# Performance work log

Measured on AMD Instinct MI355X. Metric: run time of the kernel, lower is better.

Reference implementation:

```python
import jax, jax.numpy as jnp
import numpy as np

B, T, C = 8, 512, 2048          # batch streams, qlen, hidden_size
H, Z = 32, 64                   # num_heads, head_size; A = H*Z = attention_hidden_size
A = H * Z
TMX, TDX = 32, 64               # TIME_MIX_EXTRA_DIM, TIME_DECAY_EXTRA_DIM
EPS = 1e-5 * 8.0**2             # ln_x eps = 1e-5 * head_size_divisor**2


def setup_inputs() -> dict:
    key = jax.random.key(0)
    ks = jax.random.split(key, 24)
    def rn(i, shape, scale=1.0):
        return jax.random.normal(ks[i], shape, jnp.float32) * scale
    inv_c = 1.0 / np.sqrt(C)
    return {
        "hidden_states": rn(0, (B * T, C)),
        "positions": jnp.zeros((B * T,), jnp.int32),
        "input_kv_state": jnp.zeros((B, H, Z, Z), jnp.float32),
        "input_shift_state": rn(1, (B, C)),
        "time_maa_x": rn(2, (1, 1, C), 0.1),
        "time_maa_w": rn(3, (1, 1, C), 0.1),
        "time_maa_k": rn(4, (1, 1, C), 0.1),
        "time_maa_v": rn(5, (1, 1, C), 0.1),
        "time_maa_r": rn(6, (1, 1, C), 0.1),
        "time_maa_g": rn(7, (1, 1, C), 0.1),
        "time_maa_w1": rn(8, (C, TMX * 5), inv_c),
        "time_maa_w2": rn(9, (5, TMX, C), 1.0 / np.sqrt(TMX)),
        "time_decay": rn(10, (1, 1, A), 0.5),
        "time_decay_w1": rn(11, (C, TDX), inv_c),
        "time_decay_w2": rn(12, (TDX, A), 0.01),
        "time_faaaa": rn(13, (H, Z), 0.1),
        "W_r": rn(14, (C, A), inv_c),
        "W_k": rn(15, (C, A), inv_c),
        "W_v": rn(16, (C, A), inv_c),
        "W_g": rn(17, (C, A), inv_c),
        "W_o": rn(18, (A, C), inv_c),
        "ln_w": 1.0 + rn(19, (C,), 0.1),
        "ln_b": rn(20, (C,), 0.1),
    }


def _rwkv6_forward(hidden_states, positions, input_kv_state, input_shift_state,
                   time_maa_x, time_maa_w, time_maa_k, time_maa_v, time_maa_r,
                   time_maa_g, time_maa_w1, time_maa_w2, time_decay,
                   time_decay_w1, time_decay_w2, time_faaaa,
                   W_r, W_k, W_v, W_g, W_o, ln_w, ln_b):
    x = hidden_states.reshape(B, T, C)
    pos0_is_zero = positions.reshape(B, T)[:, 0] == 0
    reset = jnp.where(pos0_is_zero, -100.0, 0.0)  # [B]
    # kill shift state for fresh sequences (matches * exp(-100))
    shift = input_shift_state * jnp.exp(reset)[:, None]  # [B, C]

    # token-shift mixing (shift state broadcast over T, as in source)
    xx = shift[:, None, :] - x  # [B, T, C]
    xxx = x + xx * time_maa_x
    mix = jnp.tanh(xxx @ time_maa_w1).reshape(B, T, 5, TMX)
    mix = jnp.einsum('btfe,fec->fbtc', mix, time_maa_w2)  # [5, B, T, C]
    mw, mk, mv, mr, mg = mix

    td_in = x + xx * (time_maa_w + mw)
    kx = x + xx * (time_maa_k + mk)
    vx = x + xx * (time_maa_v + mv)
    rx = x + xx * (time_maa_r + mr)
    gx = x + xx * (time_maa_g + mg)

    r = rx @ W_r
    k = kx @ W_k
    v = vx @ W_v
    g = jax.nn.silu(gx @ W_g)  # [B, T, A]

    w = time_decay + jnp.tanh(td_in @ time_decay_w1) @ time_decay_w2
    w = -jnp.exp(w.astype(jnp.float32))  # log-decay, [B, T, A]

    # split heads -> [T, B, H, Z] for scan
    def to_tbhz(a):
        return a.reshape(B, T, H, Z).transpose(1, 0, 2, 3)
    r_s, k_s, v_s, w_s = to_tbhz(r), to_tbhz(k), to_tbhz(v), to_tbhz(w)
    # zero out carried state at t=0 for fresh sequences
    w_s = w_s.at[0].add(reset[:, None, None])

    u = time_faaaa  # [H, Z]

    def step(S, rkvw):
        # S: [B, H, K, V] (key-dim x value-dim state)
        r_t, k_t, v_t, w_t = rkvw  # each [B, H, Z]
        kv = k_t[..., :, None] * v_t[..., None, :]  # [B, H, K, V]
        o = jnp.einsum('bhk,bhkv->bhv', r_t, S + u[None, :, :, None] * kv)
        S = jnp.exp(w_t)[..., None] * S + kv
        return S, o

    S_out, o = jax.lax.scan(step, input_kv_state, (r_s, k_s, v_s, w_s))
    xo = o.transpose(1, 0, 2, 3).reshape(B * T, C)  # [B*T, C]

    # GroupNorm over heads (num_groups = H)
    xg = xo.reshape(B * T, H, Z)
    mu = xg.mean(-1, keepdims=True)
    var = xg.var(-1, keepdims=True)
    xn = ((xg - mu) * jax.lax.rsqrt(var + EPS)).reshape(B * T, C) * ln_w + ln_b

    out = (xn.reshape(B, T, C) * g) @ W_o  # [B, T, C]
    return out.reshape(B * T, C)


def reference(hidden_states, positions, input_kv_state, input_shift_state,
              time_maa_x, time_maa_w, time_maa_k, time_maa_v, time_maa_r,
              time_maa_g, time_maa_w1, time_maa_w2, time_decay,
              time_decay_w1, time_decay_w2, time_faaaa,
              W_r, W_k, W_v, W_g, W_o, ln_w, ln_b):
    return _rwkv6_forward(hidden_states, positions, input_kv_state,
                          input_shift_state, time_maa_x, time_maa_w,
                          time_maa_k, time_maa_v, time_maa_r, time_maa_g,
                          time_maa_w1, time_maa_w2, time_decay, time_decay_w1,
                          time_decay_w2, time_faaaa, W_r, W_k, W_v, W_g, W_o,
                          ln_w, ln_b)
```

## Files before the change

### kernel.cpp

```cpp
#include <hip/hip_runtime.h>
#include <cmath>

#define NB 8
#define NT 512
#define NC 2048
#define NH 32
#define NZ 64
static constexpr float GN_EPS = 1e-5f * 64.0f;

typedef _Float16 f16;
typedef __attribute__((ext_vector_type(8))) _Float16 f16x8;
typedef __attribute__((ext_vector_type(4))) _Float16 f16x4;
typedef __attribute__((ext_vector_type(4))) float f4;

static __device__ __forceinline__ void gload16(const void* gp, void* lp) {
  __builtin_amdgcn_global_load_lds(
      (const __attribute__((address_space(1))) void*)gp,
      (__attribute__((address_space(3))) void*)lp, 16, 0, 0);
}

__global__ void k_transpose_cast(const float* __restrict__ in, f16* __restrict__ out,
                                 int R, int Cc) {
  __shared__ float tile[32][33];
  int c0 = blockIdx.x * 32, r0 = blockIdx.y * 32;
  int tx = threadIdx.x, ty = threadIdx.y;
#pragma unroll
  for (int i = 0; i < 4; ++i)
    tile[ty + i * 8][tx] = in[(size_t)(r0 + ty + i * 8) * Cc + c0 + tx];
  __syncthreads();
#pragma unroll
  for (int i = 0; i < 4; ++i)
    out[(size_t)(c0 + ty + i * 8) * R + r0 + tx] = (f16)tile[tx][ty + i * 8];
}

__global__ void k_transpose_split(const float* __restrict__ in, f16* __restrict__ ohi,
                                  f16* __restrict__ olo, int R, int Cc) {
  __shared__ float tile[32][33];
  int c0 = blockIdx.x * 32, r0 = blockIdx.y * 32;
  int tx = threadIdx.x, ty = threadIdx.y;
#pragma unroll
  for (int i = 0; i < 4; ++i)
    tile[ty + i * 8][tx] = in[(size_t)(r0 + ty + i * 8) * Cc + c0 + tx];
  __syncthreads();
#pragma unroll
  for (int i = 0; i < 4; ++i) {
    float v = tile[tx][ty + i * 8];
    f16 h = (f16)v;
    size_t o = (size_t)(c0 + ty + i * 8) * R + r0 + tx;
    ohi[o] = h;
    olo[o] = (f16)(v - (float)h);
  }
}

__global__ void k_xxx(const float* __restrict__ hs, const float* __restrict__ shift_st,
                      const int* __restrict__ positions, const float* __restrict__ maa_x,
                      float* __restrict__ xxx) {
  int i = blockIdx.x * blockDim.x + threadIdx.x;
  int idx = i * 4;
  int c = idx & (NC - 1);
  int t = idx >> 11;
  int b = t >> 9;
  float er = (positions[b * NT] == 0) ? expf(-100.0f) : 1.0f;
  const float4 x = *(const float4*)(hs + idx);
  const float4 sh = *(const float4*)(shift_st + b * NC + c);
  const float4 mx = *(const float4*)(maa_x + c);
  float4 o;
  o.x = x.x + (sh.x * er - x.x) * mx.x;
  o.y = x.y + (sh.y * er - x.y) * mx.y;
  o.z = x.z + (sh.z * er - x.z) * mx.z;
  o.w = x.w + (sh.w * er - x.w) * mx.w;
  *(float4*)(xxx + idx) = o;
}

static __device__ __forceinline__ void split4(const float4 v, int base, f16x8& hi, f16x8& lo) {
  float x[4] = {v.x, v.y, v.z, v.w};
#pragma unroll
  for (int j = 0; j < 4; ++j) {
    f16 h = (f16)x[j];
    hi[base + j] = h;
    lo[base + j] = (f16)(x[j] - (float)h);
  }
}

__global__ __launch_bounds__(64) void k_mix1_split(const float* __restrict__ A,
                                                   const f16* __restrict__ Bhi,
                                                   const f16* __restrict__ Blo,
                                                   float* __restrict__ out) {
  int m0 = blockIdx.x * 16, n0 = blockIdx.y * 16;
  int lane = threadIdx.x, lr = lane & 15, kq = lane >> 4;
  f4 acc = {0.f, 0.f, 0.f, 0.f};
  const float* ap = A + (size_t)(m0 + lr) * 2048 + kq * 8;
  const f16* bh0 = Bhi + (size_t)(n0 + lr) * 2048 + kq * 8;
  const f16* bl0 = Blo + (size_t)(n0 + lr) * 2048 + kq * 8;
  for (int k0 = 0; k0 < 2048; k0 += 32) {
    f16x8 ah, al;
    split4(*(const float4*)(ap + k0), 0, ah, al);
    split4(*(const float4*)(ap + k0 + 4), 4, ah, al);
    f16x8 bh = *(const f16x8*)(bh0 + k0);
    f16x8 bl = *(const f16x8*)(bl0 + k0);
    acc = __builtin_amdgcn_mfma_f32_16x16x32_f16(ah, bh, acc, 0, 0, 0);
    acc = __builtin_amdgcn_mfma_f32_16x16x32_f16(ah, bl, acc, 0, 0, 0);
    acc = __builtin_amdgcn_mfma_f32_16x16x32_f16(al, bh, acc, 0, 0, 0);
  }
#pragma unroll
  for (int r = 0; r < 4; ++r)
    out[(size_t)(m0 + kq * 4 + r) * 160 + n0 + lr] = tanhf(acc[r]);
}

__global__ __launch_bounds__(64) void k_tmp5_split(const float* __restrict__ mixb,
    const f16* __restrict__ Bhi, const f16* __restrict__ Blo,
    const float* __restrict__ hs, const float* __restrict__ shift_st,
    const int* __restrict__ positions,
    const float* __restrict__ maa_w, const float* __restrict__ maa_k,
    const float* __restrict__ maa_v, const float* __restrict__ maa_r,
    const float* __restrict__ maa_g,
    float* __restrict__ tdin, f16* __restrict__ kx, f16* __restrict__ vx,
    f16* __restrict__ rx, f16* __restrict__ gx) {
  int m0 = blockIdx.x * 16, n0 = blockIdx.y * 16;
  int lane = threadIdx.x, lr = lane & 15, kq = lane >> 4;
  f4 acc[5];
#pragma unroll
  for (int f = 0; f < 5; ++f) acc[f] = (f4){0.f, 0.f, 0.f, 0.f};
  const float* ap = mixb + (size_t)(m0 + lr) * 160 + kq * 8;
#pragma unroll
  for (int f = 0; f < 5; ++f) {
    f16x8 ah, al;
    split4(*(const float4*)(ap + f * 32), 0, ah, al);
    split4(*(const float4*)(ap + f * 32 + 4), 4, ah, al);
    size_t bi = ((size_t)f * 2048 + n0 + lr) * 32 + kq * 8;
    f16x8 bh = *(const f16x8*)(Bhi + bi);
    f16x8 bl = *(const f16x8*)(Blo + bi);
    acc[f] = __builtin_amdgcn_mfma_f32_16x16x32_f16(ah, bh, acc[f], 0, 0, 0);
    acc[f] = __builtin_amdgcn_mfma_f32_16x16x32_f16(ah, bl, acc[f], 0, 0, 0);
    acc[f] = __builtin_amdgcn_mfma_f32_16x16x32_f16(al, bh, acc[f], 0, 0, 0);
  }
  int c = n0 + lr;
  float mw = maa_w[c], mk = maa_k[c], mv = maa_v[c], mr = maa_r[c], mg = maa_g[c];
#pragma unroll
  for (int r = 0; r < 4; ++r) {
    int t = m0 + kq * 4 + r;
    int b = t >> 9;
    float er = (positions[b * NT] == 0) ? expf(-100.0f) : 1.0f;
    float x = hs[(size_t)t * NC + c];
    float xxv = shift_st[b * NC + c] * er - x;
    size_t oi = (size_t)t * NC + c;
    tdin[oi] = x + xxv * (mw + acc[0][r]);
    kx[oi] = (f16)(x + xxv * (mk + acc[1][r]));
    vx[oi] = (f16)(x + xxv * (mv + acc[2][r]));
    rx[oi] = (f16)(x + xxv * (mr + acc[3][r]));
    gx[oi] = (f16)(x + xxv * (mg + acc[4][r]));
  }
}

__global__ __launch_bounds__(64) void k_wd1_split(const float* __restrict__ A,
                                                  const f16* __restrict__ Bhi,
                                                  const f16* __restrict__ Blo,
                                                  float* __restrict__ out) {
  int m0 = blockIdx.x * 16, n0 = blockIdx.y * 16;
  int lane = threadIdx.x, lr = lane & 15, kq = lane >> 4;
  f4 acc = {0.f, 0.f, 0.f, 0.f};
  const float* ap = A + (size_t)(m0 + lr) * 2048 + kq * 8;
  const f16* bh0 = Bhi + (size_t)(n0 + lr) * 2048 + kq * 8;
  const f16* bl0 = Blo + (size_t)(n0 + lr) * 2048 + kq * 8;
  for (int k0 = 0; k0 < 2048; k0 += 32) {
    f16x8 ah, al;
    split4(*(const float4*)(ap + k0), 0, ah, al);
    split4(*(const float4*)(ap + k0 + 4), 4, ah, al);
    f16x8 bh = *(const f16x8*)(bh0 + k0);
    f16x8 bl = *(const f16x8*)(bl0 + k0);
    acc = __builtin_amdgcn_mfma_f32_16x16x32_f16(ah, bh, acc, 0, 0, 0);
    acc = __builtin_amdgcn_mfma_f32_16x16x32_f16(ah, bl, acc, 0, 0, 0);
    acc = __builtin_amdgcn_mfma_f32_16x16x32_f16(al, bh, acc, 0, 0, 0);
  }
#pragma unroll
  for (int r = 0; r < 4; ++r)
    out[(size_t)(m0 + kq * 4 + r) * 64 + n0 + lr] = tanhf(acc[r]);
}

__global__ __launch_bounds__(64) void k_wdecay_split(const float* __restrict__ A,
                                                     const f16* __restrict__ Bhi,
                                                     const f16* __restrict__ Blo,
                                                     const float* __restrict__ time_decay,
                                                     float* __restrict__ wout) {
  int m0 = blockIdx.x * 16, n0 = blockIdx.y * 16;
  int lane = threadIdx.x, lr = lane & 15, kq = lane >> 4;
  f4 acc = {0.f, 0.f, 0.f, 0.f};
#pragma unroll
  for (int kk = 0; kk < 2; ++kk) {
    f16x8 ah, al;
    const float* ap = A + (size_t)(m0 + lr) * 64 + kk * 32 + kq * 8;
    split4(*(const float4*)ap, 0, ah, al);
    split4(*(const float4*)(ap + 4), 4, ah, al);
    size_t bi = (size_t)(n0 + lr) * 64 + kk * 32 + kq * 8;
    f16x8 bh = *(const f16x8*)(Bhi + bi);
    f16x8 bl = *(const f16x8*)(Blo + bi);
    acc = __builtin_amdgcn_mfma_f32_16x16x32_f16(ah, bh, acc, 0, 0, 0);
    acc = __builtin_amdgcn_mfma_f32_16x16x32_f16(ah, bl, acc, 0, 0, 0);
    acc = __builtin_amdgcn_mfma_f32_16x16x32_f16(al, bh, acc, 0, 0, 0);
  }
  int c = n0 + lr;
  float td = time_decay[c];
#pragma unroll
  for (int r = 0; r < 4; ++r) {
    int t = m0 + kq * 4 + r;
    wout[(size_t)t * NC + c] = -expf(td + acc[r]);
  }
}

#define GBM 128
#define GBN 128
#define GBK 64

template <int EPI>
__global__ __launch_bounds__(256) void k_gemm_big(const f16* __restrict__ A,
                                                  const f16* __restrict__ Bt,
                                                  float* __restrict__ Cf,
                                                  f16* __restrict__ Cb, int K) {
  __shared__ __align__(16) f16 As[2][GBM][GBK];
  __shared__ __align__(16) f16 Bs[2][GBN][GBK];
  int nwg = gridDim.x * gridDim.y;
  int wg = blockIdx.y * gridDim.x + blockIdx.x;
  int swz = (wg & 7) * (nwg >> 3) + (wg >> 3);
  int n0 = (swz % gridDim.x) * GBN;
  int m0 = (swz / gridDim.x) * GBM;
  int tid = threadIdx.x;
  int wid = tid >> 6, lane = tid & 63;
  int wr = wid >> 1, wc = wid & 1;
  int lr = lane & 15, kq = lane >> 4;
  int sw = lr & 7;
  int gunit = (lane & 7) ^ (lane >> 3);
  const f16* aL = A + (size_t)(m0 + wid * 32 + (lane >> 3)) * K + gunit * 8;
  const f16* bL = Bt + (size_t)(n0 + wid * 32 + (lane >> 3)) * K + gunit * 8;
  f4 acc[4][4];
#pragma unroll
  for (int m = 0; m < 4; ++m)
#pragma unroll
    for (int n = 0; n < 4; ++n) acc[m][n] = (f4){0.f, 0.f, 0.f, 0.f};

#pragma unroll
  for (int i = 0; i < 4; ++i) {
    gload16(aL + (size_t)i * 8 * K, &As[0][wid * 32 + i * 8][0]);
    gload16(bL + (size_t)i * 8 * K, &Bs[0][wid * 32 + i * 8][0]);
  }
  __syncthreads();
  int niter = K / GBK;
  int cur = 0;
  for (int it = 0; it < niter; ++it) {
    if (it + 1 < niter) {
      int k0 = (it + 1) * GBK;
#pragma unroll
      for (int i = 0; i < 4; ++i) {
        gload16(aL + k0 + (size_t)i * 8 * K, &As[cur ^ 1][wid * 32 + i * 8][0]);
        gload16(bL + k0 + (size_t)i * 8 * K, &Bs[cur ^ 1][wid * 32 + i * 8][0]);
      }
    }
#pragma unroll
    for (int kk = 0; kk < 2; ++kk) {
      f16x8 af[4], bfv[4];
      int un = ((kk * 4 + kq) ^ sw) * 8;
#pragma unroll
      for (int m = 0; m < 4; ++m)
        af[m] = *(const f16x8*)&As[cur][wr * 64 + m * 16 + lr][un];
#pragma unroll
      for (int n = 0; n < 4; ++n)
        bfv[n] = *(const f16x8*)&Bs[cur][wc * 64 + n * 16 + lr][un];
#pragma unroll
      for (int m = 0; m < 4; ++m)
#pragma unroll
        for (int n = 0; n < 4; ++n)
          acc[m][n] = __builtin_amdgcn_mfma_f32_16x16x32_f16(af[m], bfv[n], acc[m][n], 0, 0, 0);
    }
    __syncthreads();
    cur ^= 1;
  }
#pragma unroll
  for (int m = 0; m < 4; ++m) {
    int row0 = m0 + wr * 64 + m * 16 + kq * 4;
#pragma unroll
    for (int n = 0; n < 4; ++n) {
      int col = n0 + wc * 64 + n * 16 + lr;
#pragma unroll
      for (int r = 0; r < 4; ++r) {
        float v = acc[m][n][r];
        size_t oi = (size_t)(row0 + r) * NC + col;
        if (EPI == 0) {
          Cf[oi] = v;
        } else {
          float s = v / (1.0f + expf(-v));
          Cb[oi] = (f16)s;
        }
      }
    }
  }
}

__global__ __launch_bounds__(64) void k_scanB(
    const float* rb, const float* __restrict__ kb,
    const float* __restrict__ vb, const float* __restrict__ wb,
    const float* __restrict__ kvstate, const int* __restrict__ positions,
    const float* __restrict__ faaaa, f16* __restrict__ o,
    float* rtil, float* __restrict__ Ebuf, float* __restrict__ Dbuf) {
  int blk = blockIdx.x;
  int bh = blk >> 3, c = blk & 7;
  int b = bh >> 5, h = bh & 31;
  int zz = threadIdx.x;
  __shared__ __align__(16) float shR[64];
  __shared__ __align__(16) float shE[64];
  __shared__ __align__(16) float shK[64];
  float S[64];
  if (c == 0) {
    const float* S0 = kvstate + (size_t)bh * 4096;
#pragma unroll
    for (int j = 0; j < 64; ++j) S[j] = S0[j * 64 + zz];
  } else {
#pragma unroll
    for (int j = 0; j < 64; ++j) S[j] = 0.f;
  }
  float u = faaaa[h * 64 + zz];
  float reset = (positions[b * NT] == 0) ? -100.0f : 0.0f;
  const size_t base = ((size_t)(b * NT) + c * 64) * NC + h * 64 + zz;
  float vr = rb[base], vk = kb[base], vw = wb[base], vv = vb[base];
  float Pw = 1.0f;
  for (int t = 0; t < 64; ++t) {
    float nr = 0.f, nk = 0.f, nw = 0.f, nv = 0.f;
    if (t + 1 < 64) {
      size_t idx = base + (size_t)(t + 1) * NC;
      nr = rb[idx]; nk = kb[idx]; nw = wb[idx]; nv = vb[idx];
    }
    float ww = vw;
    if (c == 0 && t == 0) ww += reset;
    float ew = expf(ww);
    shR[zz] = vr; shE[zz] = ew; shK[zz] = vk;
    float q = vr * u * vk;
    q += __shfl_xor(q, 1);  q += __shfl_xor(q, 2);  q += __shfl_xor(q, 4);
    q += __shfl_xor(q, 8);  q += __shfl_xor(q, 16); q += __shfl_xor(q, 32);
    __syncthreads();
    if (c > 0) rtil[base + (size_t)t * NC] = vr * Pw;
    Pw *= ew;
    float oacc = vv * q;
#pragma unroll
    for (int k0 = 0; k0 < 64; k0 += 4) {
      f4 r4 = *(const f4*)&shR[k0];
      f4 e4 = *(const f4*)&shE[k0];
      f4 k4 = *(const f4*)&shK[k0];
#pragma unroll
      for (int j = 0; j < 4; ++j) {
        oacc = fmaf(r4[j], S[k0 + j], oacc);
        S[k0 + j] = fmaf(e4[j], S[k0 + j], k4[j] * vv);
      }
    }
    o[base + (size_t)t * NC] = (f16)oacc;
    __syncthreads();
    vr = nr; vk = nk; vw = nw; vv = nv;
  }
  if (c < 7) {
    float* E = Ebuf + ((size_t)bh * 7 + c) * 4096;
#pragma unroll
    for (int j = 0; j < 64; ++j) E[j * 64 + zz] = S[j];
  }
  Dbuf[((size_t)bh * 8 + c) * 64 + zz] = Pw;
}

__global__ __launch_bounds__(256) void k_comb(float* __restrict__ Ebuf,
                                              const float* __restrict__ Dbuf) {
  int bh = blockIdx.x, tid = threadIdx.x;
  int k = tid >> 2, v0 = (tid & 3) * 16;
  float* base = Ebuf + (size_t)bh * 7 * 4096;
  float S[16];
#pragma unroll
  for (int j = 0; j < 16; ++j) S[j] = base[k * 64 + v0 + j];
  for (int c = 2; c <= 7; ++c) {
    float d = Dbuf[((size_t)bh * 8 + (c - 1)) * 64 + k];
    float* slot = base + (size_t)(c - 1) * 4096;
#pragma unroll
    for (int j = 0; j < 16; ++j) {
      S[j] = fmaf(d, S[j], slot[k * 64 + v0 + j]);
      slot[k * 64 + v0 + j] = S[j];
    }
  }
}

__global__ __launch_bounds__(256) void k_fix(const float* __restrict__ rtil,
                                             const float* __restrict__ Ebuf,
                                             f16* __restrict__ o) {
  int blk = blockIdx.x;
  int bh = blk / 7, cm = blk - bh * 7;
  int c = cm + 1;
  int b = bh >> 5, h = bh & 31;
  __shared__ float Rs[64][65];
  __shared__ float Ss[64][65];
  int tid = threadIdx.x;
  const float* rsrc = rtil + ((size_t)(b * NT) + c * 64) * NC + h * NZ;
  const float* ssrc = Ebuf + ((size_t)bh * 7 + cm) * 4096;
#pragma unroll
  for (int q = 0; q < 4; ++q) {
    int li = tid * 4 + q;
    int rr = li >> 4, cc = (li & 15) * 4;
    float4 x = *(const float4*)(rsrc + (size_t)rr * NC + cc);
    Rs[rr][cc] = x.x; Rs[rr][cc + 1] = x.y; Rs[rr][cc + 2] = x.z; Rs[rr][cc + 3] = x.w;
    float4 y = *(const float4*)(ssrc + rr * 64 + cc);
    Ss[rr][cc] = y.x; Ss[rr][cc + 1] = y.y; Ss[rr][cc + 2] = y.z; Ss[rr][cc + 3] = y.w;
  }
  __syncthreads();
  int t = tid >> 2, v0 = (tid & 3) * 16;
  float acc[16];
#pragma unroll
  for (int j = 0; j < 16; ++j) acc[j] = 0.f;
  for (int k = 0; k < 64; ++k) {
    float rv = Rs[t][k];
#pragma unroll
    for (int j = 0; j < 16; ++j) acc[j] = fmaf(rv, Ss[k][v0 + j], acc[j]);
  }
  f16* op = o + ((size_t)(b * NT) + c * 64 + t) * NC + h * NZ + v0;
  f16x8 o0 = *(f16x8*)op, o1 = *(f16x8*)(op + 8);
#pragma unroll
  for (int j = 0; j < 8; ++j) {
    o0[j] = (f16)((float)o0[j] + acc[j]);
    o1[j] = (f16)((float)o1[j] + acc[j + 8]);
  }
  *(f16x8*)op = o0;
  *(f16x8*)(op + 8) = o1;
}

__global__ __launch_bounds__(256) void k_gnorm(const f16* __restrict__ xo, const f16* __restrict__ g,
    const float* __restrict__ ln_w, const float* __restrict__ ln_b, f16* __restrict__ y) {
  int t = blockIdx.x;
  int tid = threadIdx.x;
  int c = tid * 8;
  f16x8 xv8 = *(const f16x8*)(xo + (size_t)t * NC + c);
  float xv[8];
#pragma unroll
  for (int j = 0; j < 8; ++j) xv[j] = (float)xv8[j];
  float s = 0.f, ss = 0.f;
#pragma unroll
  for (int j = 0; j < 8; ++j) { s += xv[j]; ss += xv[j] * xv[j]; }
  s += __shfl_xor(s, 1); ss += __shfl_xor(ss, 1);
  s += __shfl_xor(s, 2); ss += __shfl_xor(ss, 2);
  s += __shfl_xor(s, 4); ss += __shfl_xor(ss, 4);
  float mu = s * (1.0f / 64.0f);
  float var = ss * (1.0f / 64.0f) - mu * mu;
  float rstd = rsqrtf(var + GN_EPS);
  f16x8 gv = *(const f16x8*)(g + (size_t)t * NC + c);
  f16x8 ov;
#pragma unroll
  for (int j = 0; j < 8; ++j) {
    float xn = (xv[j] - mu) * rstd * ln_w[c + j] + ln_b[c + j];
    ov[j] = (f16)(xn * (float)gv[j]);
  }
  *(f16x8*)(y + (size_t)t * NC + c) = ov;
}

extern "C" void kernel_launch(void* const* d_in, const int* in_sizes, int n_in,
                              void* d_out, int out_size, void* d_ws, size_t ws_size,
                              hipStream_t stream) {
  const float* hs = (const float*)d_in[0];
  const int* positions = (const int*)d_in[1];
  const float* kvstate = (const float*)d_in[2];
  const float* shift_st = (const float*)d_in[3];
  const float* maa_x = (const float*)d_in[4];
  const float* maa_w = (const float*)d_in[5];
  const float* maa_k = (const float*)d_in[6];
  const float* maa_v = (const float*)d_in[7];
  const float* maa_r = (const float*)d_in[8];
  const float* maa_g = (const float*)d_in[9];
  const float* maa_w1 = (const float*)d_in[10];
  const float* maa_w2 = (const float*)d_in[11];
  const float* time_decay = (const float*)d_in[12];
  const float* decay_w1 = (const float*)d_in[13];
  const float* decay_w2 = (const float*)d_in[14];
  const float* faaaa = (const float*)d_in[15];
  const float* W_r = (const float*)d_in[16];
  const float* W_k = (const float*)d_in[17];
  const float* W_v = (const float*)d_in[18];
  const float* W_g = (const float*)d_in[19];
  const float* W_o = (const float*)d_in[20];
  const float* ln_w = (const float*)d_in[21];
  const float* ln_b = (const float*)d_in[22];

  char* ws = (char*)d_ws;
  size_t off = 0;
  auto alloc = [&](size_t n) {
    char* p = ws + off;
    off += (n + 255) & ~(size_t)255;
    return p;
  };
  f16* w1t_hi = (f16*)alloc(160ull * 2048 * 2);
  f16* w1t_lo = (f16*)alloc(160ull * 2048 * 2);
  f16* w2t_hi = (f16*)alloc(5ull * 2048 * 32 * 2);
  f16* w2t_lo = (f16*)alloc(5ull * 2048 * 32 * 2);
  f16* dw1t_hi = (f16*)alloc(64ull * 2048 * 2);
  f16* dw1t_lo = (f16*)alloc(64ull * 2048 * 2);
  f16* dw2t_hi = (f16*)alloc(2048ull * 64 * 2);
  f16* dw2t_lo = (f16*)alloc(2048ull * 64 * 2);
  float* mixb = (float*)alloc(4096ull * 160 * 4);
  float* wd1 = (float*)alloc(4096ull * 64 * 4);
  char* R_A = alloc(4096ull * 2048 * 4);
  char* R_B = alloc(4096ull * 2048 * 4);
  char* R_C = alloc(4096ull * 2048 * 4);
  char* R_D = alloc(4096ull * 2048 * 4);
  char* R_E = alloc(4096ull * 2048 * 2);
  char* F12 = alloc(4096ull * 2048 * 4);
  char* F3 = alloc(4096ull * 2048 * 2);
  char* F4 = alloc(4096ull * 2048 * 2);

  float* xxx = (float*)R_A;
  float* tdin = (float*)R_A;
  float* wbuf = (float*)R_A;
  float* rbuf = (float*)R_B;
  float* kbuf = (float*)R_C;
  float* vbuf = (float*)R_D;
  f16* wstage = (f16*)R_E;
  f16* obuf = (f16*)R_E;
  f16* kx = (f16*)F12;
  f16* vx = (f16*)(F12 + 4096ull * 2048 * 2);
  float* Ebuf = (float*)F12;
  float* Dbuf = (float*)(F12 + 29360128);
  f16* rx = (f16*)F3;
  f16* gbuf = (f16*)F3;
  f16* gx = (f16*)F4;
  f16* wt_o = (f16*)F4;

  dim3 tb(32, 8);
  k_transpose_split<<<dim3(5, 64), tb, 0, stream>>>(maa_w1, w1t_hi, w1t_lo, 2048, 160);
  for (int f = 0; f < 5; ++f)
    k_transpose_split<<<dim3(64, 1), tb, 0, stream>>>(maa_w2 + (size_t)f * 32 * 2048,
        w2t_hi + (size_t)f * 2048 * 32, w2t_lo + (size_t)f * 2048 * 32, 32, 2048);
  k_transpose_split<<<dim3(2, 64), tb, 0, stream>>>(decay_w1, dw1t_hi, dw1t_lo, 2048, 64);
  k_transpose_split<<<dim3(64, 2), tb, 0, stream>>>(decay_w2, dw2t_hi, dw2t_lo, 64, 2048);

  k_xxx<<<8192, 256, 0, stream>>>(hs, shift_st, positions, maa_x, xxx);
  k_mix1_split<<<dim3(256, 10), 64, 0, stream>>>(xxx, w1t_hi, w1t_lo, mixb);
  k_tmp5_split<<<dim3(256, 128), 64, 0, stream>>>(mixb, w2t_hi, w2t_lo, hs, shift_st,
      positions, maa_w, maa_k, maa_v, maa_r, maa_g, tdin, kx, vx, rx, gx);
  k_wd1_split<<<dim3(256, 4), 64, 0, stream>>>(tdin, dw1t_hi, dw1t_lo, wd1);
  k_wdecay_split<<<dim3(256, 128), 64, 0, stream>>>(wd1, dw2t_hi, dw2t_lo, time_decay, wbuf);

  dim3 gg(2048 / GBN, 4096 / GBM);
  k_transpose_cast<<<dim3(64, 64), tb, 0, stream>>>(W_r, wstage, 2048, 2048);
  k_gemm_big<0><<<gg, 256, 0, stream>>>(rx, wstage, rbuf, nullptr, 2048);
  k_transpose_cast<<<dim3(64, 64), tb, 0, stream>>>(W_k, wstage, 2048, 2048);
  k_gemm_big<0><<<gg, 256, 0, stream>>>(kx, wstage, kbuf, nullptr, 2048);
  k_transpose_cast<<<dim3(64, 64), tb, 0, stream>>>(W_v, wstage, 2048, 2048);
  k_gemm_big<0><<<gg, 256, 0, stream>>>(vx, wstage, vbuf, nullptr, 2048);
  k_transpose_cast<<<dim3(64, 64), tb, 0, stream>>>(W_g, wstage, 2048, 2048);
  k_gemm_big<2><<<gg, 256, 0, stream>>>(gx, wstage, nullptr, gbuf, 2048);
  k_transpose_cast<<<dim3(64, 64), tb, 0, stream>>>(W_o, wt_o, 2048, 2048);

  k_scanB<<<2048, 64, 0, stream>>>(rbuf, kbuf, vbuf, wbuf, kvstate, positions, faaaa,
                                   obuf, rbuf, Ebuf, Dbuf);
  k_comb<<<256, 256, 0, stream>>>(Ebuf, Dbuf);
  k_fix<<<1792, 256, 0, stream>>>(rbuf, Ebuf, obuf);

  k_gnorm<<<4096, 256, 0, stream>>>(obuf, gbuf, ln_w, ln_b, obuf);
  k_gemm_big<0><<<gg, 256, 0, stream>>>(obuf, wt_o, (float*)d_out, nullptr, 2048);
}
```

Before: 654.6 us.

## Split scan state across two wavefronts and merge w2 transpose launches

The chunked WKV scan kernel now runs two 64-lane wavefronts per block. Each wavefront holds half of the 64x64 state rows, and the wavefronts divide the r/k and w/v loads between them. Partial outputs are combined through shared memory, which halves per-thread state registers and the serial FMA work per step. The cost is an extra shared-memory exchange per timestep. Separately, five launches of the w2 transpose-split are folded into one launch using a z-grid dimension, which cuts launch overhead.

```diff
diff --git a/kernel.cpp b/kernel.cpp
--- a/kernel.cpp
+++ b/kernel.cpp
@@ -47,6 +47,29 @@
     float v = tile[tx][ty + i * 8];
     f16 h = (f16)v;
     size_t o = (size_t)(c0 + ty + i * 8) * R + r0 + tx;
+    ohi[o] = h;
+    olo[o] = (f16)(v - (float)h);
+  }
+}
+
+__global__ void k_tsplit_w2(const float* __restrict__ in0, f16* __restrict__ ohi0,
+                            f16* __restrict__ olo0) {
+  __shared__ float tile[32][33];
+  int f = blockIdx.z;
+  const float* in = in0 + (size_t)f * 32 * 2048;
+  f16* ohi = ohi0 + (size_t)f * 2048 * 32;
+  f16* olo = olo0 + (size_t)f * 2048 * 32;
+  int c0 = blockIdx.x * 32;
+  int tx = threadIdx.x, ty = threadIdx.y;
+#pragma unroll
+  for (int i = 0; i < 4; ++i)
+    tile[ty + i * 8][tx] = in[(size_t)(ty + i * 8) * 2048 + c0 + tx];
+  __syncthreads();
+#pragma unroll
+  for (int i = 0; i < 4; ++i) {
+    float v = tile[tx][ty + i * 8];
+    f16 h = (f16)v;
+    size_t o = (size_t)(c0 + ty + i * 8) * 32 + tx;
     ohi[o] = h;
     olo[o] = (f16)(v - (float)h);
   }
@@ -294,7 +317,7 @@
   }
 }
 
-__global__ __launch_bounds__(64) void k_scanB(
+__global__ __launch_bounds__(128) void k_scanC(
     const float* rb, const float* __restrict__ kb,
     const float* __restrict__ vb, const float* __restrict__ wb,
     const float* __restrict__ kvstate, const int* __restrict__ positions,
@@ -303,62 +326,83 @@
   int blk = blockIdx.x;
   int bh = blk >> 3, c = blk & 7;
   int b = bh >> 5, h = bh & 31;
-  int zz = threadIdx.x;
+  int tid = threadIdx.x;
+  int w = tid >> 6, zz = tid & 63;
   __shared__ __align__(16) float shR[64];
   __shared__ __align__(16) float shE[64];
   __shared__ __align__(16) float shK[64];
-  float S[64];
+  __shared__ __align__(16) float shV[64];
+  __shared__ __align__(16) float opart[64];
+  float S[32];
   if (c == 0) {
     const float* S0 = kvstate + (size_t)bh * 4096;
 #pragma unroll
-    for (int j = 0; j < 64; ++j) S[j] = S0[j * 64 + zz];
+    for (int j = 0; j < 32; ++j) S[j] = S0[(w * 32 + j) * 64 + zz];
   } else {
 #pragma unroll
-    for (int j = 0; j < 64; ++j) S[j] = 0.f;
+    for (int j = 0; j < 32; ++j) S[j] = 0.f;
   }
   float u = faaaa[h * 64 + zz];
   float reset = (positions[b * NT] == 0) ? -100.0f : 0.0f;
   const size_t base = ((size_t)(b * NT) + c * 64) * NC + h * 64 + zz;
-  float vr = rb[base], vk = kb[base], vw = wb[base], vv = vb[base];
+  float a_cur, b_cur;
+  if (w == 0) { a_cur = rb[base]; b_cur = kb[base]; }
+  else        { a_cur = wb[base]; b_cur = vb[base]; }
   float Pw = 1.0f;
   for (int t = 0; t < 64; ++t) {
-    float nr = 0.f, nk = 0.f, nw = 0.f, nv = 0.f;
+    float a_nxt = 0.f, b_nxt = 0.f;
     if (t + 1 < 64) {
       size_t idx = base + (size_t)(t + 1) * NC;
-      nr = rb[idx]; nk = kb[idx]; nw = wb[idx]; nv = vb[idx];
-    }
-    float ww = vw;
-    if (c == 0 && t == 0) ww += reset;
-    float ew = expf(ww);
-    shR[zz] = vr; shE[zz] = ew; shK[zz] = vk;
-    float q = vr * u * vk;
-    q += __shfl_xor(q, 1);  q += __shfl_xor(q, 2);  q += __shfl_xor(q, 4);
-    q += __shfl_xor(q, 8);  q += __shfl_xor(q, 16); q += __shfl_xor(q, 32);
+      if (w == 0) { a_nxt = rb[idx]; b_nxt = kb[idx]; }
+      else        { a_nxt = wb[idx]; b_nxt = vb[idx]; }
+    }
+    float ew = 0.f;
+    if (w == 0) {
+      shR[zz] = a_cur;
+      shK[zz] = b_cur;
+    } else {
+      float ww = a_cur;
+      if (c == 0 && t == 0) ww += reset;
+      ew = expf(ww);
+      shE[zz] = ew;
+      shV[zz] = b_cur;
+    }
     __syncthreads();
-    if (c > 0) rtil[base + (size_t)t * NC] = vr * Pw;
-    Pw *= ew;
-    float oacc = vv * q;
-#pragma unroll
-    for (int k0 = 0; k0 < 64; k0 += 4) {
-      f4 r4 = *(const f4*)&shR[k0];
-      f4 e4 = *(const f4*)&shE[k0];
-      f4 k4 = *(const f4*)&shK[k0];
+    float vv = shV[zz];
+    float oacc = 0.f;
+    int kb0 = w * 32;
+#pragma unroll
+    for (int k0 = 0; k0 < 32; k0 += 4) {
+      f4 r4 = *(const f4*)&shR[kb0 + k0];
+      f4 e4 = *(const f4*)&shE[kb0 + k0];
+      f4 k4 = *(const f4*)&shK[kb0 + k0];
 #pragma unroll
       for (int j = 0; j < 4; ++j) {
         oacc = fmaf(r4[j], S[k0 + j], oacc);
         S[k0 + j] = fmaf(e4[j], S[k0 + j], k4[j] * vv);
       }
     }
-    o[base + (size_t)t * NC] = (f16)oacc;
+    float q = 0.f;
+    if (w == 0) {
+      q = a_cur * u * b_cur;
+      q += __shfl_xor(q, 1);  q += __shfl_xor(q, 2);  q += __shfl_xor(q, 4);
+      q += __shfl_xor(q, 8);  q += __shfl_xor(q, 16); q += __shfl_xor(q, 32);
+    } else {
+      if (c > 0) rtil[base + (size_t)t * NC] = shR[zz] * Pw;
+      Pw *= ew;
+      opart[zz] = oacc;
+    }
     __syncthreads();
-    vr = nr; vk = nk; vw = nw; vv = nv;
+    if (w == 0)
+      o[base + (size_t)t * NC] = (f16)(oacc + opart[zz] + vv * q);
+    a_cur = a_nxt; b_cur = b_nxt;
   }
   if (c < 7) {
     float* E = Ebuf + ((size_t)bh * 7 + c) * 4096;
 #pragma unroll
-    for (int j = 0; j < 64; ++j) E[j * 64 + zz] = S[j];
-  }
-  Dbuf[((size_t)bh * 8 + c) * 64 + zz] = Pw;
+    for (int j = 0; j < 32; ++j) E[(w * 32 + j) * 64 + zz] = S[j];
+  }
+  if (w == 1) Dbuf[((size_t)bh * 8 + c) * 64 + zz] = Pw;
 }
 
 __global__ __launch_bounds__(256) void k_comb(float* __restrict__ Ebuf,
@@ -522,9 +566,7 @@
 
   dim3 tb(32, 8);
   k_transpose_split<<<dim3(5, 64), tb, 0, stream>>>(maa_w1, w1t_hi, w1t_lo, 2048, 160);
-  for (int f = 0; f < 5; ++f)
-    k_transpose_split<<<dim3(64, 1), tb, 0, stream>>>(maa_w2 + (size_t)f * 32 * 2048,
-        w2t_hi + (size_t)f * 2048 * 32, w2t_lo + (size_t)f * 2048 * 32, 32, 2048);
+  k_tsplit_w2<<<dim3(64, 1, 5), tb, 0, stream>>>(maa_w2, w2t_hi, w2t_lo);
   k_transpose_split<<<dim3(2, 64), tb, 0, stream>>>(decay_w1, dw1t_hi, dw1t_lo, 2048, 64);
   k_transpose_split<<<dim3(64, 2), tb, 0, stream>>>(decay_w2, dw2t_hi, dw2t_lo, 64, 2048);
 
@@ -546,8 +588,8 @@
   k_gemm_big<2><<<gg, 256, 0, stream>>>(gx, wstage, nullptr, gbuf, 2048);
   k_transpose_cast<<<dim3(64, 64), tb, 0, stream>>>(W_o, wt_o, 2048, 2048);
 
-  k_scanB<<<2048, 64, 0, stream>>>(rbuf, kbuf, vbuf, wbuf, kvstate, positions, faaaa,
-                                   obuf, rbuf, Ebuf, Dbuf);
+  k_scanC<<<2048, 128, 0, stream>>>(rbuf, kbuf, vbuf, wbuf, kvstate, positions, faaaa,
+                                    obuf, rbuf, Ebuf, Dbuf);
   k_comb<<<256, 256, 0, stream>>>(Ebuf, Dbuf);
   k_fix<<<1792, 256, 0, stream>>>(rbuf, Ebuf, obuf);
 
```

Result: slower. 694.3 us (+6.1%).

## Prefetch two K-tiles ahead in big GEMM with vmcnt waits; batch w2 transposes

Applied to the files above, without the earlier changes.

The big GEMM main loop now issues loads for two tiles ahead and uses explicit s_waitcnt vmcnt counts plus raw s_barrier, in place of __syncthreads after each tile. This gives more overlap between global-to-LDS loads and MFMA work. Separately, the five small maa_w2 transpose-split launches are merged into one launch over a z-dimension, which cuts launch overhead. Hand-written waitcnt counts are fragile and depend on how many loads the compiler emits per stage.

```diff
diff --git a/kernel.cpp b/kernel.cpp
--- a/kernel.cpp
+++ b/kernel.cpp
@@ -47,6 +47,29 @@
     float v = tile[tx][ty + i * 8];
     f16 h = (f16)v;
     size_t o = (size_t)(c0 + ty + i * 8) * R + r0 + tx;
+    ohi[o] = h;
+    olo[o] = (f16)(v - (float)h);
+  }
+}
+
+__global__ void k_tsplit_w2(const float* __restrict__ in0, f16* __restrict__ ohi0,
+                            f16* __restrict__ olo0) {
+  __shared__ float tile[32][33];
+  int f = blockIdx.z;
+  const float* in = in0 + (size_t)f * 32 * 2048;
+  f16* ohi = ohi0 + (size_t)f * 2048 * 32;
+  f16* olo = olo0 + (size_t)f * 2048 * 32;
+  int c0 = blockIdx.x * 32;
+  int tx = threadIdx.x, ty = threadIdx.y;
+#pragma unroll
+  for (int i = 0; i < 4; ++i)
+    tile[ty + i * 8][tx] = in[(size_t)(ty + i * 8) * 2048 + c0 + tx];
+  __syncthreads();
+#pragma unroll
+  for (int i = 0; i < 4; ++i) {
+    float v = tile[tx][ty + i * 8];
+    f16 h = (f16)v;
+    size_t o = (size_t)(c0 + ty + i * 8) * 32 + tx;
     ohi[o] = h;
     olo[o] = (f16)(v - (float)h);
   }
@@ -237,23 +260,26 @@
 #pragma unroll
     for (int n = 0; n < 4; ++n) acc[m][n] = (f4){0.f, 0.f, 0.f, 0.f};
 
-#pragma unroll
-  for (int i = 0; i < 4; ++i) {
-    gload16(aL + (size_t)i * 8 * K, &As[0][wid * 32 + i * 8][0]);
-    gload16(bL + (size_t)i * 8 * K, &Bs[0][wid * 32 + i * 8][0]);
-  }
-  __syncthreads();
+  auto stage = [&](int buf, int t) {
+    int k0 = t * GBK;
+#pragma unroll
+    for (int i = 0; i < 4; ++i) {
+      gload16(aL + k0 + (size_t)i * 8 * K, &As[buf][wid * 32 + i * 8][0]);
+      gload16(bL + k0 + (size_t)i * 8 * K, &Bs[buf][wid * 32 + i * 8][0]);
+    }
+  };
+
   int niter = K / GBK;
-  int cur = 0;
+  stage(0, 0);
+  stage(1, 1);
   for (int it = 0; it < niter; ++it) {
-    if (it + 1 < niter) {
-      int k0 = (it + 1) * GBK;
-#pragma unroll
-      for (int i = 0; i < 4; ++i) {
-        gload16(aL + k0 + (size_t)i * 8 * K, &As[cur ^ 1][wid * 32 + i * 8][0]);
-        gload16(bL + k0 + (size_t)i * 8 * K, &Bs[cur ^ 1][wid * 32 + i * 8][0]);
-      }
-    }
+    if (it == niter - 1)
+      asm volatile("s_waitcnt vmcnt(0)" ::: "memory");
+    else
+      asm volatile("s_waitcnt vmcnt(8)" ::: "memory");
+    __builtin_amdgcn_sched_barrier(0);
+    __builtin_amdgcn_s_barrier();
+    int cur = it & 1;
 #pragma unroll
     for (int kk = 0; kk < 2; ++kk) {
       f16x8 af[4], bfv[4];
@@ -270,8 +296,8 @@
         for (int n = 0; n < 4; ++n)
           acc[m][n] = __builtin_amdgcn_mfma_f32_16x16x32_f16(af[m], bfv[n], acc[m][n], 0, 0, 0);
     }
-    __syncthreads();
-    cur ^= 1;
+    __builtin_amdgcn_s_barrier();
+    if (it + 2 < niter) stage(cur, it + 2);
   }
 #pragma unroll
   for (int m = 0; m < 4; ++m) {
@@ -522,9 +548,7 @@
 
   dim3 tb(32, 8);
   k_transpose_split<<<dim3(5, 64), tb, 0, stream>>>(maa_w1, w1t_hi, w1t_lo, 2048, 160);
-  for (int f = 0; f < 5; ++f)
-    k_transpose_split<<<dim3(64, 1), tb, 0, stream>>>(maa_w2 + (size_t)f * 32 * 2048,
-        w2t_hi + (size_t)f * 2048 * 32, w2t_lo + (size_t)f * 2048 * 32, 32, 2048);
+  k_tsplit_w2<<<dim3(64, 1, 5), tb, 0, stream>>>(maa_w2, w2t_hi, w2t_lo);
   k_transpose_split<<<dim3(2, 64), tb, 0, stream>>>(decay_w1, dw1t_hi, dw1t_lo, 2048, 64);
   k_transpose_split<<<dim3(64, 2), tb, 0, stream>>>(decay_w2, dw2t_hi, dw2t_lo, 64, 2048);
 
```

After: 639.9 us. -2.3%, faster.
